# Performance work log

Measured on AMD Instinct MI355X. Metric: run time of the kernel, lower is better.

## Reference

```python
import math
import jax, jax.numpy as jnp
import numpy as np

B, T, T_P, C, H = 4, 2048, 256, 768, 12
HD = C // H


def setup_inputs() -> dict:
    key = jax.random.key(0)
    k1, k2, k3, k4 = jax.random.split(key, 4)
    x = jax.random.normal(k1, (B, T, C), dtype=jnp.float32)
    prefix = jax.random.normal(k2, (B, T_P, C), dtype=jnp.float32)
    # torch nn.Linear weight layout: (out_features, in_features)
    W_qkv = jax.random.normal(k3, (3 * C, C), dtype=jnp.float32) * (1.0 / math.sqrt(C))
    W_out = jax.random.normal(k4, (C, C), dtype=jnp.float32) * (1.0 / math.sqrt(C))
    return {"x": x, "prefix": prefix, "W_qkv": W_qkv, "W_out": W_out}


def _mac_causal_mask(t_p: int, t: int) -> jnp.ndarray:
    total = t_p + t
    mask = jnp.zeros((total, total), dtype=bool)
    mask = mask.at[:t_p, t_p:].set(True)  # h tokens blocked from x tokens
    causal = jnp.triu(jnp.ones((t, t), dtype=bool), k=1)  # causal within x block
    return mask.at[t_p:, t_p:].set(causal)


def reference(x, prefix, W_qkv, W_out):
    b, t, c = x.shape
    t_p = prefix.shape[1]
    t_all = t_p + t
    x_full = jnp.concatenate([prefix, x], axis=1)          # (B, T_all, C)
    qkv = x_full @ W_qkv.T                                  # (B, T_all, 3C)
    q, k, v = jnp.split(qkv, 3, axis=-1)
    # (B, H, T_all, HD)
    q = q.reshape(b, t_all, H, HD).transpose(0, 2, 1, 3)
    k = k.reshape(b, t_all, H, HD).transpose(0, 2, 1, 3)
    v = v.reshape(b, t_all, H, HD).transpose(0, 2, 1, 3)
    scale = 1.0 / math.sqrt(HD)
    att = jnp.einsum('bhqd,bhkd->bhqk', q, k) * scale       # (B, H, T_all, T_all)
    mask = _mac_causal_mask(t_p, t)
    att = jnp.where(mask[None, None], -jnp.inf, att)
    att = jax.nn.softmax(att, axis=-1)                      # dropout = identity (eval)
    out = jnp.einsum('bhqk,bhkd->bhqd', att, v)             # (B, H, T_all, HD)
    out = out.transpose(0, 2, 1, 3).reshape(b, t_all, c)
    out = out @ W_out.T
    return out[:, t_p:, :]                                  # only x portion (B, T, C)
```

## Files before the change

### kernel.cpp

```cpp
#include <hip/hip_runtime.h>

constexpr int Bn   = 4;
constexpr int Tn   = 2048;
constexpr int TPn  = 256;
constexpr int TALLn = 2304;
constexpr int Cn   = 768;
constexpr int Hn   = 12;
constexpr int HDn  = 64;

typedef __bf16 bf16x4 __attribute__((ext_vector_type(4)));
typedef __bf16 bf16x8 __attribute__((ext_vector_type(8)));
typedef float  f32x4  __attribute__((ext_vector_type(4)));
typedef unsigned u32x4 __attribute__((ext_vector_type(4)));

__device__ __forceinline__ unsigned short f2bf(float f) {
    unsigned int x = __float_as_uint(f);
    x += 0x7fffu + ((x >> 16) & 1u);
    return (unsigned short)(x >> 16);
}

__device__ __forceinline__ unsigned cvt_pk_bf16(float a, float b) {
    unsigned r;
    asm("v_cvt_pk_bf16_f32 %0, %1, %2" : "=v"(r) : "v"(a), "v"(b));
    return r;
}

#define ASYNC16(gsrc, ldst)                                                           \
    __builtin_amdgcn_global_load_lds((__attribute__((address_space(1))) void*)(gsrc), \
                                     (__attribute__((address_space(3))) void*)(ldst), \
                                     16, 0, 0)

__global__ __launch_bounds__(256) void k_build_xfull(
        const float* __restrict__ x, const float* __restrict__ pre,
        unsigned short* __restrict__ xf) {
    int idx = blockIdx.x * 256 + threadIdx.x;
    int row = idx / (Cn / 4);
    int c   = (idx - row * (Cn / 4)) * 4;
    int b = row / TALLn, tt = row - b * TALLn;
    const float* src = (tt < TPn) ? pre + ((size_t)b * TPn + tt) * Cn + c
                                  : x   + ((size_t)b * Tn + (tt - TPn)) * Cn + c;
    float4 f = *reinterpret_cast<const float4*>(src);
    ushort4 o = { f2bf(f.x), f2bf(f.y), f2bf(f.z), f2bf(f.w) };
    *reinterpret_cast<ushort4*>(xf + (size_t)row * Cn + c) = o;
}

__global__ __launch_bounds__(256) void k_cast2(
        const float* __restrict__ wqkv, const float* __restrict__ wout,
        unsigned short* __restrict__ wqb, unsigned short* __restrict__ wob) {
    int idx = (blockIdx.x * 256 + threadIdx.x) * 4;
    const int n1 = 3 * Cn * Cn;
    const float* src;
    unsigned short* dst;
    if (idx < n1) { src = wqkv + idx; dst = wqb + idx; }
    else          { src = wout + (idx - n1); dst = wob + (idx - n1); }
    float4 f = *reinterpret_cast<const float4*>(src);
    ushort4 o = { f2bf(f.x), f2bf(f.y), f2bf(f.z), f2bf(f.w) };
    *reinterpret_cast<ushort4*>(dst) = o;
}

__global__ __launch_bounds__(256) void k_qkv_gemm(
        const unsigned short* __restrict__ A, const unsigned short* __restrict__ W,
        unsigned short* __restrict__ Qb, unsigned short* __restrict__ Kb,
        unsigned short* __restrict__ Vt) {
    __shared__ __align__(16) unsigned short smem[16384];
    const int tid  = threadIdx.x;
    const int wave = tid >> 6;
    const int lane = tid & 63;
    const int g = lane >> 4, l16 = lane & 15;
    const int m0 = blockIdx.x * 128, n0 = blockIdx.y * 128;
    const int wr = wave >> 1, wc = wave & 1;

    const unsigned short* pa[2];
    const unsigned short* pb[2];
    int sd[2];
    #pragma unroll
    for (int inst = 0; inst < 2; ++inst) {
        const int li = inst * 256 + tid;
        const int row = li >> 2;
        const int ch = (li & 3) ^ ((row >> 1) & 3);
        pa[inst] = A + (size_t)(m0 + row) * Cn + ch * 8;
        pb[inst] = W + (size_t)(n0 + row) * Cn + ch * 8;
        sd[inst] = (inst * 256 + wave * 64) * 8;
    }
    int aoff[4], boff[4];
    #pragma unroll
    for (int mt = 0; mt < 4; ++mt) {
        const int ra = wr * 64 + mt * 16 + l16;
        aoff[mt] = ra * 32 + ((g ^ ((ra >> 1) & 3)) << 3);
        const int rb = wc * 64 + mt * 16 + l16;
        boff[mt] = rb * 32 + ((g ^ ((rb >> 1) & 3)) << 3);
    }

    f32x4 acc[4][4] = {};

    #pragma unroll
    for (int inst = 0; inst < 2; ++inst) {
        ASYNC16(pa[inst], &smem[0]    + sd[inst]);
        ASYNC16(pb[inst], &smem[8192] + sd[inst]);
        pa[inst] += 32;
        pb[inst] += 32;
    }
    __syncthreads();

    int buf = 0;
    for (int kk = 0; kk < 24; ++kk) {
        if (kk + 1 < 24) {
            #pragma unroll
            for (int inst = 0; inst < 2; ++inst) {
                ASYNC16(pa[inst], &smem[(buf ^ 1) * 4096]        + sd[inst]);
                ASYNC16(pb[inst], &smem[8192 + (buf ^ 1) * 4096] + sd[inst]);
                pa[inst] += 32;
                pb[inst] += 32;
            }
        }
        const unsigned short* Ab = &smem[buf * 4096];
        const unsigned short* Bb = &smem[8192 + buf * 4096];
        bf16x8 af[4], bfv[4];
        #pragma unroll
        for (int mt = 0; mt < 4; ++mt) {
            af[mt]  = *reinterpret_cast<const bf16x8*>(&Ab[aoff[mt]]);
            bfv[mt] = *reinterpret_cast<const bf16x8*>(&Bb[boff[mt]]);
        }
        __builtin_amdgcn_s_setprio(1);
        #pragma unroll
        for (int mt = 0; mt < 4; ++mt)
            #pragma unroll
            for (int nt = 0; nt < 4; ++nt)
                acc[mt][nt] = __builtin_amdgcn_mfma_f32_16x16x32_bf16(
                        af[mt], bfv[nt], acc[mt][nt], 0, 0, 0);
        __builtin_amdgcn_s_setprio(0);
        buf ^= 1;
        __syncthreads();
    }

    const int b   = m0 / TALLn;
    const int t0  = m0 - b * TALLn;
    const int sel = n0 / Cn;
    const int hn0 = n0 - sel * Cn;
    constexpr float SCQ = 0.18033688011112042f;

    if (sel == 2) {
        #pragma unroll
        for (int mt = 0; mt < 4; ++mt)
            #pragma unroll
            for (int nt = 0; nt < 4; ++nt)
                #pragma unroll
                for (int r = 0; r < 4; ++r) {
                    const int t  = wr * 64 + mt * 16 + g * 4 + r;
                    const int hn = wc * 64 + nt * 16 + l16;
                    smem[hn * 128 + (((t >> 3) ^ (hn & 7)) << 3) + (t & 7)] =
                            f2bf(acc[mt][nt][r]);
                }
        __syncthreads();
        #pragma unroll
        for (int j = 0; j < 8; ++j) {
            const int u  = tid + 256 * j;
            const int hn = u >> 4, tc = u & 15;
            const int tile64 = tc >> 3;
            const int np = tc & 7;
            const int kg = np >> 2, gs = np & 3;
            const int tgA = tile64 * 8 + kg * 4 + (gs >> 1);
            const int sub = (gs & 1) * 4;
            bf16x4 rA = *reinterpret_cast<const bf16x4*>(
                    &smem[hn * 128 + ((tgA ^ (hn & 7)) << 3) + sub]);
            bf16x4 rB = *reinterpret_cast<const bf16x4*>(
                    &smem[hn * 128 + (((tgA + 2) ^ (hn & 7)) << 3) + sub]);
            bf16x8 v = __builtin_shufflevector(rA, rB, 0, 1, 2, 3, 4, 5, 6, 7);
            const int hh = (hn0 + hn) >> 6;
            const int dd = hn & 63;
            *reinterpret_cast<bf16x8*>(
                    &Vt[(((size_t)b * Hn + hh) * HDn + dd) * TALLn + t0 + tc * 8]) = v;
        }
    } else {
        #pragma unroll
        for (int mt = 0; mt < 4; ++mt)
            #pragma unroll
            for (int nt = 0; nt < 4; ++nt)
                #pragma unroll
                for (int r = 0; r < 4; ++r) {
                    const int t  = t0 + wr * 64 + mt * 16 + g * 4 + r;
                    const int hn = hn0 + wc * 64 + nt * 16 + l16;
                    const int h = hn >> 6, d = hn & 63;
                    if (sel == 0)
                        Qb[(((size_t)b * Hn + h) * TALLn + t) * HDn + d] =
                                f2bf(acc[mt][nt][r] * SCQ);
                    else
                        Kb[(((size_t)b * Hn + h) * TALLn + t) * HDn + d] =
                                f2bf(acc[mt][nt][r]);
                }
    }
}

__global__ __launch_bounds__(256) void k_attn(
        const unsigned short* __restrict__ Qb, const unsigned short* __restrict__ Kb,
        const unsigned short* __restrict__ Vt, unsigned short* __restrict__ Ob) {
    __shared__ __align__(16) unsigned short Ks[2][4096];
    __shared__ __align__(16) unsigned short Vs[2][4096];
    const int tid  = threadIdx.x;
    const int wq   = tid >> 6;
    const int lane = tid & 63;
    const int l16  = lane & 15;
    const int g    = lane >> 4;

    const int fb  = blockIdx.x;
    const int j   = fb >> 3;
    const int bh  = 6 * (fb & 7) + (j % 6);
    const int chunk = 31 - (j / 6);
    const int nkt = 5 + chunk;
    const size_t kv = (size_t)bh * TALLn * HDn;

    int koff[4][2];
    #pragma unroll
    for (int band = 0; band < 4; ++band)
        #pragma unroll
        for (int ks = 0; ks < 2; ++ks)
            koff[band][ks] = (band * 16 + l16) * 64 + (((ks * 4 + g) ^ (l16 & 7)) << 3);
    int voff[2];
    #pragma unroll
    for (int kg = 0; kg < 2; ++kg)
        voff[kg] = l16 * 64 + (((kg * 4 + g) ^ (l16 & 7)) << 3);
    const unsigned short* pk[2];
    const unsigned short* pv[2];
    int sdst[2];
    #pragma unroll
    for (int inst = 0; inst < 2; ++inst) {
        const int li = inst * 256 + tid;
        const int row = li >> 3;
        const int ch = (li & 7) ^ (row & 7);
        pk[inst] = Kb + kv + row * HDn + ch * 8;
        pv[inst] = Vt + kv + row * TALLn + ch * 8;
        sdst[inst] = (inst * 256 + wq * 64) * 8;
    }
    constexpr int KSTRIDE = 64 * HDn;
    constexpr int VSTRIDE = 64;

    bf16x8 qf[2];
    {
        const int tq = TPn + chunk * 64 + wq * 16 + l16;
        #pragma unroll
        for (int ks = 0; ks < 2; ++ks)
            qf[ks] = *reinterpret_cast<const bf16x8*>(
                    Qb + kv + (size_t)tq * HDn + ks * 32 + g * 8);
    }

    bf16x8 ones;
    #pragma unroll
    for (int i = 0; i < 8; ++i) ones[i] = (__bf16)1.0f;

    f32x4 oacc[4] = {};
    f32x4 lacc = {};

    #pragma unroll
    for (int inst = 0; inst < 2; ++inst) {
        ASYNC16(pk[inst], &Ks[0][0] + sdst[inst]);
        ASYNC16(pv[inst], &Vs[0][0] + sdst[inst]);
        pk[inst] += KSTRIDE;
        pv[inst] += VSTRIDE;
    }
    __syncthreads();

    int buf = 0;
    for (int t = 0; t < nkt; ++t) {
        if (t + 1 < nkt) {
            #pragma unroll
            for (int inst = 0; inst < 2; ++inst) {
                ASYNC16(pk[inst], &Ks[buf ^ 1][0] + sdst[inst]);
                ASYNC16(pv[inst], &Vs[buf ^ 1][0] + sdst[inst]);
                pk[inst] += KSTRIDE;
                pv[inst] += VSTRIDE;
            }
        }
        const unsigned short* Ksb = &Ks[buf][0];
        const unsigned short* Vsb = &Vs[buf][0];

        f32x4 sacc[4] = {};
        __builtin_amdgcn_s_setprio(1);
        #pragma unroll
        for (int band = 0; band < 4; ++band) {
            bf16x8 k0 = *reinterpret_cast<const bf16x8*>(&Ksb[koff[band][0]]);
            bf16x8 k1 = *reinterpret_cast<const bf16x8*>(&Ksb[koff[band][1]]);
            sacc[band] = __builtin_amdgcn_mfma_f32_16x16x32_bf16(
                    k0, qf[0], sacc[band], 0, 0, 0);
            sacc[band] = __builtin_amdgcn_mfma_f32_16x16x32_bf16(
                    k1, qf[1], sacc[band], 0, 0, 0);
        }
        __builtin_amdgcn_s_setprio(0);

        if (t == nkt - 1) {
            const int lim = TPn + chunk * 64 + wq * 16 + l16 - t * 64;
            #pragma unroll
            for (int band = 0; band < 4; ++band)
                #pragma unroll
                for (int r = 0; r < 4; ++r)
                    sacc[band][r] = (band * 16 + g * 4 + r <= lim) ? sacc[band][r]
                                                                   : -1e30f;
        }
        unsigned dwb[4][2];
        #pragma unroll
        for (int band = 0; band < 4; ++band) {
            const float e0 = exp2f(sacc[band][0]);
            const float e1 = exp2f(sacc[band][1]);
            const float e2 = exp2f(sacc[band][2]);
            const float e3 = exp2f(sacc[band][3]);
            dwb[band][0] = cvt_pk_bf16(e0, e1);
            dwb[band][1] = cvt_pk_bf16(e2, e3);
        }

        __builtin_amdgcn_s_setprio(1);
        #pragma unroll
        for (int kg = 0; kg < 2; ++kg) {
            const u32x4 uu = { dwb[2 * kg][0], dwb[2 * kg][1],
                               dwb[2 * kg + 1][0], dwb[2 * kg + 1][1] };
            const bf16x8 pf = __builtin_bit_cast(bf16x8, uu);
            lacc = __builtin_amdgcn_mfma_f32_16x16x32_bf16(ones, pf, lacc, 0, 0, 0);
            #pragma unroll
            for (int dband = 0; dband < 4; ++dband) {
                bf16x8 vf = *reinterpret_cast<const bf16x8*>(
                        &Vsb[dband * 1024 + voff[kg]]);
                oacc[dband] = __builtin_amdgcn_mfma_f32_16x16x32_bf16(
                        vf, pf, oacc[dband], 0, 0, 0);
            }
        }
        __builtin_amdgcn_s_setprio(0);

        buf ^= 1;
        __syncthreads();
    }

    const int b = bh / Hn, h = bh - b * Hn;
    const float inv = 1.0f / lacc[0];
    const size_t row = (size_t)b * Tn + chunk * 64 + wq * 16 + l16;
    #pragma unroll
    for (int dband = 0; dband < 4; ++dband) {
        ushort4 st;
        st.x = f2bf(oacc[dband][0] * inv);
        st.y = f2bf(oacc[dband][1] * inv);
        st.z = f2bf(oacc[dband][2] * inv);
        st.w = f2bf(oacc[dband][3] * inv);
        *reinterpret_cast<ushort4*>(&Ob[row * Cn + h * 64 + dband * 16 + g * 4]) = st;
    }
}

__global__ __launch_bounds__(256) void k_out_gemm(
        const unsigned short* __restrict__ A, const unsigned short* __restrict__ W,
        float* __restrict__ out) {
    __shared__ __align__(16) unsigned short smem[16384];
    const int tid  = threadIdx.x;
    const int wave = tid >> 6;
    const int lane = tid & 63;
    const int g = lane >> 4, l16 = lane & 15;
    const int m0 = blockIdx.x * 128, n0 = blockIdx.y * 128;
    const int wr = wave >> 1, wc = wave & 1;

    const unsigned short* pa[2];
    const unsigned short* pb[2];
    int sd[2];
    #pragma unroll
    for (int inst = 0; inst < 2; ++inst) {
        const int li = inst * 256 + tid;
        const int row = li >> 2;
        const int ch = (li & 3) ^ ((row >> 1) & 3);
        pa[inst] = A + (size_t)(m0 + row) * Cn + ch * 8;
        pb[inst] = W + (size_t)(n0 + row) * Cn + ch * 8;
        sd[inst] = (inst * 256 + wave * 64) * 8;
    }
    int aoff[4], boff[4];
    #pragma unroll
    for (int mt = 0; mt < 4; ++mt) {
        const int ra = wr * 64 + mt * 16 + l16;
        aoff[mt] = ra * 32 + ((g ^ ((ra >> 1) & 3)) << 3);
        const int rb = wc * 64 + mt * 16 + l16;
        boff[mt] = rb * 32 + ((g ^ ((rb >> 1) & 3)) << 3);
    }

    f32x4 acc[4][4] = {};

    #pragma unroll
    for (int inst = 0; inst < 2; ++inst) {
        ASYNC16(pa[inst], &smem[0]    + sd[inst]);
        ASYNC16(pb[inst], &smem[8192] + sd[inst]);
        pa[inst] += 32;
        pb[inst] += 32;
    }
    __syncthreads();

    int buf = 0;
    for (int kk = 0; kk < 24; ++kk) {
        if (kk + 1 < 24) {
            #pragma unroll
            for (int inst = 0; inst < 2; ++inst) {
                ASYNC16(pa[inst], &smem[(buf ^ 1) * 4096]        + sd[inst]);
                ASYNC16(pb[inst], &smem[8192 + (buf ^ 1) * 4096] + sd[inst]);
                pa[inst] += 32;
                pb[inst] += 32;
            }
        }
        const unsigned short* Ab = &smem[buf * 4096];
        const unsigned short* Bb = &smem[8192 + buf * 4096];
        bf16x8 af[4], bfv[4];
        #pragma unroll
        for (int mt = 0; mt < 4; ++mt) {
            af[mt]  = *reinterpret_cast<const bf16x8*>(&Ab[aoff[mt]]);
            bfv[mt] = *reinterpret_cast<const bf16x8*>(&Bb[boff[mt]]);
        }
        __builtin_amdgcn_s_setprio(1);
        #pragma unroll
        for (int mt = 0; mt < 4; ++mt)
            #pragma unroll
            for (int nt = 0; nt < 4; ++nt)
                acc[mt][nt] = __builtin_amdgcn_mfma_f32_16x16x32_bf16(
                        af[mt], bfv[nt], acc[mt][nt], 0, 0, 0);
        __builtin_amdgcn_s_setprio(0);
        buf ^= 1;
        __syncthreads();
    }

    #pragma unroll
    for (int mt = 0; mt < 4; ++mt)
        #pragma unroll
        for (int nt = 0; nt < 4; ++nt)
            #pragma unroll
            for (int r = 0; r < 4; ++r) {
                const int m = m0 + wr * 64 + mt * 16 + g * 4 + r;
                const int n = n0 + wc * 64 + nt * 16 + l16;
                out[(size_t)m * Cn + n] = acc[mt][nt][r];
            }
}

extern "C" void kernel_launch(void* const* d_in, const int* in_sizes, int n_in,
                              void* d_out, int out_size, void* d_ws, size_t ws_size,
                              hipStream_t stream) {
    const float* x    = (const float*)d_in[0];
    const float* pre  = (const float*)d_in[1];
    const float* wqkv = (const float*)d_in[2];
    const float* wout = (const float*)d_in[3];
    float* out = (float*)d_out;
    char* ws = (char*)d_ws;

    unsigned short* xf  = (unsigned short*)(ws + 0);
    unsigned short* wqb = (unsigned short*)(ws + 14155776);
    unsigned short* wob = (unsigned short*)(ws + 17694720);
    unsigned short* Qb  = (unsigned short*)(ws + 18874368);
    unsigned short* Kb  = (unsigned short*)(ws + 33030144);
    unsigned short* Vt  = (unsigned short*)(ws + 47185920);
    unsigned short* Ob  = (unsigned short*)(ws + 61341696);

    k_build_xfull<<<dim3((Bn * TALLn * Cn / 4) / 256), 256, 0, stream>>>(x, pre, xf);
    k_cast2<<<dim3((4 * Cn * Cn / 4) / 256), 256, 0, stream>>>(wqkv, wout, wqb, wob);
    k_qkv_gemm<<<dim3((Bn * TALLn) / 128, (3 * Cn) / 128), 256, 0, stream>>>(
            xf, wqb, Qb, Kb, Vt);
    k_attn<<<dim3(1536), 256, 0, stream>>>(Qb, Kb, Vt, Ob);
    k_out_gemm<<<dim3((Bn * Tn) / 128, Cn / 128), 256, 0, stream>>>(Ob, wob, out);
}
```

Baseline: 141.2 us.

## Merge cast kernels and give each attention wave two query tiles

The two fp32-to-bf16 cast kernels are merged into one prep launch to remove a kernel launch. The attention kernel drops from 4 waves to 2 waves per block, and each wave now handles 32 query rows as two 16-row tiles. Each K/V fragment read from LDS therefore feeds twice as many MFMAs, cutting LDS traffic per unit of compute. The cost is higher register pressure and fewer waves per block for latency hiding, plus each thread now issues twice as many async loads.

```diff
diff --git a/kernel.cpp b/kernel.cpp
--- a/kernel.cpp
+++ b/kernel.cpp
@@ -30,29 +30,28 @@
                                      (__attribute__((address_space(3))) void*)(ldst), \
                                      16, 0, 0)
 
-__global__ __launch_bounds__(256) void k_build_xfull(
+__global__ __launch_bounds__(256) void k_prep(
         const float* __restrict__ x, const float* __restrict__ pre,
-        unsigned short* __restrict__ xf) {
-    int idx = blockIdx.x * 256 + threadIdx.x;
-    int row = idx / (Cn / 4);
-    int c   = (idx - row * (Cn / 4)) * 4;
-    int b = row / TALLn, tt = row - b * TALLn;
-    const float* src = (tt < TPn) ? pre + ((size_t)b * TPn + tt) * Cn + c
-                                  : x   + ((size_t)b * Tn + (tt - TPn)) * Cn + c;
-    float4 f = *reinterpret_cast<const float4*>(src);
-    ushort4 o = { f2bf(f.x), f2bf(f.y), f2bf(f.z), f2bf(f.w) };
-    *reinterpret_cast<ushort4*>(xf + (size_t)row * Cn + c) = o;
-}
-
-__global__ __launch_bounds__(256) void k_cast2(
         const float* __restrict__ wqkv, const float* __restrict__ wout,
-        unsigned short* __restrict__ wqb, unsigned short* __restrict__ wob) {
-    int idx = (blockIdx.x * 256 + threadIdx.x) * 4;
-    const int n1 = 3 * Cn * Cn;
+        unsigned short* __restrict__ xf, unsigned short* __restrict__ wqb,
+        unsigned short* __restrict__ wob) {
+    const int idx = blockIdx.x * 256 + threadIdx.x;
+    constexpr int NXF = Bn * TALLn * Cn / 4;
+    constexpr int NW1 = 3 * Cn * Cn / 4;
     const float* src;
     unsigned short* dst;
-    if (idx < n1) { src = wqkv + idx; dst = wqb + idx; }
-    else          { src = wout + (idx - n1); dst = wob + (idx - n1); }
+    if (idx < NXF) {
+        const int row = idx / (Cn / 4);
+        const int c   = (idx - row * (Cn / 4)) * 4;
+        const int b = row / TALLn, tt = row - b * TALLn;
+        src = (tt < TPn) ? pre + ((size_t)b * TPn + tt) * Cn + c
+                         : x   + ((size_t)b * Tn + (tt - TPn)) * Cn + c;
+        dst = xf + (size_t)row * Cn + c;
+    } else {
+        const int k = idx - NXF;
+        if (k < NW1) { src = wqkv + (size_t)k * 4; dst = wqb + (size_t)k * 4; }
+        else { src = wout + (size_t)(k - NW1) * 4; dst = wob + (size_t)(k - NW1) * 4; }
+    }
     float4 f = *reinterpret_cast<const float4*>(src);
     ushort4 o = { f2bf(f.x), f2bf(f.y), f2bf(f.z), f2bf(f.w) };
     *reinterpret_cast<ushort4*>(dst) = o;
@@ -191,13 +190,13 @@
     }
 }
 
-__global__ __launch_bounds__(256) void k_attn(
+__global__ __launch_bounds__(128) void k_attn(
         const unsigned short* __restrict__ Qb, const unsigned short* __restrict__ Kb,
         const unsigned short* __restrict__ Vt, unsigned short* __restrict__ Ob) {
     __shared__ __align__(16) unsigned short Ks[2][4096];
     __shared__ __align__(16) unsigned short Vs[2][4096];
     const int tid  = threadIdx.x;
-    const int wq   = tid >> 6;
+    const int wave = tid >> 6;
     const int lane = tid & 63;
     const int l16  = lane & 15;
     const int g    = lane >> 4;
@@ -219,39 +218,42 @@
     #pragma unroll
     for (int kg = 0; kg < 2; ++kg)
         voff[kg] = l16 * 64 + (((kg * 4 + g) ^ (l16 & 7)) << 3);
-    const unsigned short* pk[2];
-    const unsigned short* pv[2];
-    int sdst[2];
-    #pragma unroll
-    for (int inst = 0; inst < 2; ++inst) {
-        const int li = inst * 256 + tid;
+    const unsigned short* pk[4];
+    const unsigned short* pv[4];
+    int sdst[4];
+    #pragma unroll
+    for (int inst = 0; inst < 4; ++inst) {
+        const int li = inst * 128 + tid;
         const int row = li >> 3;
         const int ch = (li & 7) ^ (row & 7);
         pk[inst] = Kb + kv + row * HDn + ch * 8;
         pv[inst] = Vt + kv + row * TALLn + ch * 8;
-        sdst[inst] = (inst * 256 + wq * 64) * 8;
+        sdst[inst] = (inst * 128 + wave * 64) * 8;
     }
     constexpr int KSTRIDE = 64 * HDn;
     constexpr int VSTRIDE = 64;
 
-    bf16x8 qf[2];
+    bf16x8 qfA[2], qfB[2];
     {
-        const int tq = TPn + chunk * 64 + wq * 16 + l16;
-        #pragma unroll
-        for (int ks = 0; ks < 2; ++ks)
-            qf[ks] = *reinterpret_cast<const bf16x8*>(
+        const int tq = TPn + chunk * 64 + wave * 32 + l16;
+        #pragma unroll
+        for (int ks = 0; ks < 2; ++ks) {
+            qfA[ks] = *reinterpret_cast<const bf16x8*>(
                     Qb + kv + (size_t)tq * HDn + ks * 32 + g * 8);
+            qfB[ks] = *reinterpret_cast<const bf16x8*>(
+                    Qb + kv + (size_t)(tq + 16) * HDn + ks * 32 + g * 8);
+        }
     }
 
     bf16x8 ones;
     #pragma unroll
     for (int i = 0; i < 8; ++i) ones[i] = (__bf16)1.0f;
 
-    f32x4 oacc[4] = {};
-    f32x4 lacc = {};
-
-    #pragma unroll
-    for (int inst = 0; inst < 2; ++inst) {
+    f32x4 oaccA[4] = {}, oaccB[4] = {};
+    f32x4 laccA = {}, laccB = {};
+
+    #pragma unroll
+    for (int inst = 0; inst < 4; ++inst) {
         ASYNC16(pk[inst], &Ks[0][0] + sdst[inst]);
         ASYNC16(pv[inst], &Vs[0][0] + sdst[inst]);
         pk[inst] += KSTRIDE;
@@ -263,7 +265,7 @@
     for (int t = 0; t < nkt; ++t) {
         if (t + 1 < nkt) {
             #pragma unroll
-            for (int inst = 0; inst < 2; ++inst) {
+            for (int inst = 0; inst < 4; ++inst) {
                 ASYNC16(pk[inst], &Ks[buf ^ 1][0] + sdst[inst]);
                 ASYNC16(pv[inst], &Vs[buf ^ 1][0] + sdst[inst]);
                 pk[inst] += KSTRIDE;
@@ -273,52 +275,59 @@
         const unsigned short* Ksb = &Ks[buf][0];
         const unsigned short* Vsb = &Vs[buf][0];
 
-        f32x4 sacc[4] = {};
+        f32x4 sA[4] = {}, sB[4] = {};
         __builtin_amdgcn_s_setprio(1);
         #pragma unroll
         for (int band = 0; band < 4; ++band) {
             bf16x8 k0 = *reinterpret_cast<const bf16x8*>(&Ksb[koff[band][0]]);
             bf16x8 k1 = *reinterpret_cast<const bf16x8*>(&Ksb[koff[band][1]]);
-            sacc[band] = __builtin_amdgcn_mfma_f32_16x16x32_bf16(
-                    k0, qf[0], sacc[band], 0, 0, 0);
-            sacc[band] = __builtin_amdgcn_mfma_f32_16x16x32_bf16(
-                    k1, qf[1], sacc[band], 0, 0, 0);
+            sA[band] = __builtin_amdgcn_mfma_f32_16x16x32_bf16(k0, qfA[0], sA[band], 0, 0, 0);
+            sA[band] = __builtin_amdgcn_mfma_f32_16x16x32_bf16(k1, qfA[1], sA[band], 0, 0, 0);
+            sB[band] = __builtin_amdgcn_mfma_f32_16x16x32_bf16(k0, qfB[0], sB[band], 0, 0, 0);
+            sB[band] = __builtin_amdgcn_mfma_f32_16x16x32_bf16(k1, qfB[1], sB[band], 0, 0, 0);
         }
         __builtin_amdgcn_s_setprio(0);
 
         if (t == nkt - 1) {
-            const int lim = TPn + chunk * 64 + wq * 16 + l16 - t * 64;
+            const int limA = wave * 32 + l16;
             #pragma unroll
             for (int band = 0; band < 4; ++band)
                 #pragma unroll
-                for (int r = 0; r < 4; ++r)
-                    sacc[band][r] = (band * 16 + g * 4 + r <= lim) ? sacc[band][r]
-                                                                   : -1e30f;
-        }
-        unsigned dwb[4][2];
+                for (int r = 0; r < 4; ++r) {
+                    const int key = band * 16 + g * 4 + r;
+                    sA[band][r] = (key <= limA)      ? sA[band][r] : -1e30f;
+                    sB[band][r] = (key <= limA + 16) ? sB[band][r] : -1e30f;
+                }
+        }
+
+        unsigned dwA[4][2], dwB[4][2];
         #pragma unroll
         for (int band = 0; band < 4; ++band) {
-            const float e0 = exp2f(sacc[band][0]);
-            const float e1 = exp2f(sacc[band][1]);
-            const float e2 = exp2f(sacc[band][2]);
-            const float e3 = exp2f(sacc[band][3]);
-            dwb[band][0] = cvt_pk_bf16(e0, e1);
-            dwb[band][1] = cvt_pk_bf16(e2, e3);
+            dwA[band][0] = cvt_pk_bf16(exp2f(sA[band][0]), exp2f(sA[band][1]));
+            dwA[band][1] = cvt_pk_bf16(exp2f(sA[band][2]), exp2f(sA[band][3]));
+            dwB[band][0] = cvt_pk_bf16(exp2f(sB[band][0]), exp2f(sB[band][1]));
+            dwB[band][1] = cvt_pk_bf16(exp2f(sB[band][2]), exp2f(sB[band][3]));
         }
 
         __builtin_amdgcn_s_setprio(1);
         #pragma unroll
         for (int kg = 0; kg < 2; ++kg) {
-            const u32x4 uu = { dwb[2 * kg][0], dwb[2 * kg][1],
-                               dwb[2 * kg + 1][0], dwb[2 * kg + 1][1] };
-            const bf16x8 pf = __builtin_bit_cast(bf16x8, uu);
-            lacc = __builtin_amdgcn_mfma_f32_16x16x32_bf16(ones, pf, lacc, 0, 0, 0);
+            const u32x4 uA = { dwA[2 * kg][0], dwA[2 * kg][1],
+                               dwA[2 * kg + 1][0], dwA[2 * kg + 1][1] };
+            const u32x4 uB = { dwB[2 * kg][0], dwB[2 * kg][1],
+                               dwB[2 * kg + 1][0], dwB[2 * kg + 1][1] };
+            const bf16x8 pfA = __builtin_bit_cast(bf16x8, uA);
+            const bf16x8 pfB = __builtin_bit_cast(bf16x8, uB);
+            laccA = __builtin_amdgcn_mfma_f32_16x16x32_bf16(ones, pfA, laccA, 0, 0, 0);
+            laccB = __builtin_amdgcn_mfma_f32_16x16x32_bf16(ones, pfB, laccB, 0, 0, 0);
             #pragma unroll
             for (int dband = 0; dband < 4; ++dband) {
                 bf16x8 vf = *reinterpret_cast<const bf16x8*>(
                         &Vsb[dband * 1024 + voff[kg]]);
-                oacc[dband] = __builtin_amdgcn_mfma_f32_16x16x32_bf16(
-                        vf, pf, oacc[dband], 0, 0, 0);
+                oaccA[dband] = __builtin_amdgcn_mfma_f32_16x16x32_bf16(
+                        vf, pfA, oaccA[dband], 0, 0, 0);
+                oaccB[dband] = __builtin_amdgcn_mfma_f32_16x16x32_bf16(
+                        vf, pfB, oaccB[dband], 0, 0, 0);
             }
         }
         __builtin_amdgcn_s_setprio(0);
@@ -328,16 +337,22 @@
     }
 
     const int b = bh / Hn, h = bh - b * Hn;
-    const float inv = 1.0f / lacc[0];
-    const size_t row = (size_t)b * Tn + chunk * 64 + wq * 16 + l16;
+    const float invA = 1.0f / laccA[0];
+    const float invB = 1.0f / laccB[0];
+    const size_t rowA = (size_t)b * Tn + chunk * 64 + wave * 32 + l16;
     #pragma unroll
     for (int dband = 0; dband < 4; ++dband) {
         ushort4 st;
-        st.x = f2bf(oacc[dband][0] * inv);
-        st.y = f2bf(oacc[dband][1] * inv);
-        st.z = f2bf(oacc[dband][2] * inv);
-        st.w = f2bf(oacc[dband][3] * inv);
-        *reinterpret_cast<ushort4*>(&Ob[row * Cn + h * 64 + dband * 16 + g * 4]) = st;
+        st.x = f2bf(oaccA[dband][0] * invA);
+        st.y = f2bf(oaccA[dband][1] * invA);
+        st.z = f2bf(oaccA[dband][2] * invA);
+        st.w = f2bf(oaccA[dband][3] * invA);
+        *reinterpret_cast<ushort4*>(&Ob[rowA * Cn + h * 64 + dband * 16 + g * 4]) = st;
+        st.x = f2bf(oaccB[dband][0] * invB);
+        st.y = f2bf(oaccB[dband][1] * invB);
+        st.z = f2bf(oaccB[dband][2] * invB);
+        st.w = f2bf(oaccB[dband][3] * invB);
+        *reinterpret_cast<ushort4*>(&Ob[(rowA + 16) * Cn + h * 64 + dband * 16 + g * 4]) = st;
     }
 }
 
@@ -445,10 +460,10 @@
     unsigned short* Vt  = (unsigned short*)(ws + 47185920);
     unsigned short* Ob  = (unsigned short*)(ws + 61341696);
 
-    k_build_xfull<<<dim3((Bn * TALLn * Cn / 4) / 256), 256, 0, stream>>>(x, pre, xf);
-    k_cast2<<<dim3((4 * Cn * Cn / 4) / 256), 256, 0, stream>>>(wqkv, wout, wqb, wob);
+    constexpr int PREP_UNITS = (Bn * TALLn * Cn + 4 * Cn * Cn) / 4;
+    k_prep<<<dim3(PREP_UNITS / 256), 256, 0, stream>>>(x, pre, wqkv, wout, xf, wqb, wob);
     k_qkv_gemm<<<dim3((Bn * TALLn) / 128, (3 * Cn) / 128), 256, 0, stream>>>(
             xf, wqb, Qb, Kb, Vt);
-    k_attn<<<dim3(1536), 256, 0, stream>>>(Qb, Kb, Vt, Ob);
+    k_attn<<<dim3(1536), 128, 0, stream>>>(Qb, Kb, Vt, Ob);
     k_out_gemm<<<dim3((Bn * Tn) / 128, Cn / 128), 256, 0, stream>>>(Ob, wob, out);
 }
```

Result: slower. 158.6 us (+12.3%).

## Triple-buffer attention K/V staging and merge input cast kernels

Applied to the files above, without the earlier changes.

The attention kernel moves from double to triple buffering of K/V tiles in LDS. It prefetches two tiles ahead and uses explicit vmcnt waits with a single barrier per iteration, replacing the full __syncthreads, so more global-to-LDS latency can be hidden. The two fp32-to-bf16 prep kernels are also fused into one launch to save launch overhead. The cost is more LDS per block, which may lower occupancy. The causal mask limit expression is simplified, since it is equivalent on the last tile.

```diff
diff --git a/kernel.cpp b/kernel.cpp
--- a/kernel.cpp
+++ b/kernel.cpp
@@ -30,29 +30,28 @@
                                      (__attribute__((address_space(3))) void*)(ldst), \
                                      16, 0, 0)
 
-__global__ __launch_bounds__(256) void k_build_xfull(
+__global__ __launch_bounds__(256) void k_prep(
         const float* __restrict__ x, const float* __restrict__ pre,
-        unsigned short* __restrict__ xf) {
-    int idx = blockIdx.x * 256 + threadIdx.x;
-    int row = idx / (Cn / 4);
-    int c   = (idx - row * (Cn / 4)) * 4;
-    int b = row / TALLn, tt = row - b * TALLn;
-    const float* src = (tt < TPn) ? pre + ((size_t)b * TPn + tt) * Cn + c
-                                  : x   + ((size_t)b * Tn + (tt - TPn)) * Cn + c;
-    float4 f = *reinterpret_cast<const float4*>(src);
-    ushort4 o = { f2bf(f.x), f2bf(f.y), f2bf(f.z), f2bf(f.w) };
-    *reinterpret_cast<ushort4*>(xf + (size_t)row * Cn + c) = o;
-}
-
-__global__ __launch_bounds__(256) void k_cast2(
         const float* __restrict__ wqkv, const float* __restrict__ wout,
-        unsigned short* __restrict__ wqb, unsigned short* __restrict__ wob) {
-    int idx = (blockIdx.x * 256 + threadIdx.x) * 4;
-    const int n1 = 3 * Cn * Cn;
+        unsigned short* __restrict__ xf, unsigned short* __restrict__ wqb,
+        unsigned short* __restrict__ wob) {
+    const int idx = blockIdx.x * 256 + threadIdx.x;
+    constexpr int NXF = Bn * TALLn * Cn / 4;
+    constexpr int NW1 = 3 * Cn * Cn / 4;
     const float* src;
     unsigned short* dst;
-    if (idx < n1) { src = wqkv + idx; dst = wqb + idx; }
-    else          { src = wout + (idx - n1); dst = wob + (idx - n1); }
+    if (idx < NXF) {
+        const int row = idx / (Cn / 4);
+        const int c   = (idx - row * (Cn / 4)) * 4;
+        const int b = row / TALLn, tt = row - b * TALLn;
+        src = (tt < TPn) ? pre + ((size_t)b * TPn + tt) * Cn + c
+                         : x   + ((size_t)b * Tn + (tt - TPn)) * Cn + c;
+        dst = xf + (size_t)row * Cn + c;
+    } else {
+        const int k = idx - NXF;
+        if (k < NW1) { src = wqkv + (size_t)k * 4; dst = wqb + (size_t)k * 4; }
+        else { src = wout + (size_t)(k - NW1) * 4; dst = wob + (size_t)(k - NW1) * 4; }
+    }
     float4 f = *reinterpret_cast<const float4*>(src);
     ushort4 o = { f2bf(f.x), f2bf(f.y), f2bf(f.z), f2bf(f.w) };
     *reinterpret_cast<ushort4*>(dst) = o;
@@ -194,8 +193,8 @@
 __global__ __launch_bounds__(256) void k_attn(
         const unsigned short* __restrict__ Qb, const unsigned short* __restrict__ Kb,
         const unsigned short* __restrict__ Vt, unsigned short* __restrict__ Ob) {
-    __shared__ __align__(16) unsigned short Ks[2][4096];
-    __shared__ __align__(16) unsigned short Vs[2][4096];
+    __shared__ __align__(16) unsigned short Ks[3][4096];
+    __shared__ __align__(16) unsigned short Vs[3][4096];
     const int tid  = threadIdx.x;
     const int wq   = tid >> 6;
     const int lane = tid & 63;
@@ -234,6 +233,16 @@
     constexpr int KSTRIDE = 64 * HDn;
     constexpr int VSTRIDE = 64;
 
+    auto stageKV = [&](int bs) {
+        #pragma unroll
+        for (int inst = 0; inst < 2; ++inst) {
+            ASYNC16(pk[inst], &Ks[bs][0] + sdst[inst]);
+            ASYNC16(pv[inst], &Vs[bs][0] + sdst[inst]);
+            pk[inst] += KSTRIDE;
+            pv[inst] += VSTRIDE;
+        }
+    };
+
     bf16x8 qf[2];
     {
         const int tq = TPn + chunk * 64 + wq * 16 + l16;
@@ -250,28 +259,21 @@
     f32x4 oacc[4] = {};
     f32x4 lacc = {};
 
-    #pragma unroll
-    for (int inst = 0; inst < 2; ++inst) {
-        ASYNC16(pk[inst], &Ks[0][0] + sdst[inst]);
-        ASYNC16(pv[inst], &Vs[0][0] + sdst[inst]);
-        pk[inst] += KSTRIDE;
-        pv[inst] += VSTRIDE;
-    }
-    __syncthreads();
-
-    int buf = 0;
+    stageKV(0);
+    stageKV(1);
+    asm volatile("s_waitcnt vmcnt(4)" ::: "memory");
+    __builtin_amdgcn_sched_barrier(0);
+    __builtin_amdgcn_s_barrier();
+    __builtin_amdgcn_sched_barrier(0);
+
+    int cur = 0;
     for (int t = 0; t < nkt; ++t) {
-        if (t + 1 < nkt) {
-            #pragma unroll
-            for (int inst = 0; inst < 2; ++inst) {
-                ASYNC16(pk[inst], &Ks[buf ^ 1][0] + sdst[inst]);
-                ASYNC16(pv[inst], &Vs[buf ^ 1][0] + sdst[inst]);
-                pk[inst] += KSTRIDE;
-                pv[inst] += VSTRIDE;
-            }
-        }
-        const unsigned short* Ksb = &Ks[buf][0];
-        const unsigned short* Vsb = &Vs[buf][0];
+        if (t + 2 < nkt) {
+            const int nb = (cur + 2 >= 3) ? cur - 1 : cur + 2;
+            stageKV(nb);
+        }
+        const unsigned short* Ksb = &Ks[cur][0];
+        const unsigned short* Vsb = &Vs[cur][0];
 
         f32x4 sacc[4] = {};
         __builtin_amdgcn_s_setprio(1);
@@ -287,7 +289,7 @@
         __builtin_amdgcn_s_setprio(0);
 
         if (t == nkt - 1) {
-            const int lim = TPn + chunk * 64 + wq * 16 + l16 - t * 64;
+            const int lim = wq * 16 + l16;
             #pragma unroll
             for (int band = 0; band < 4; ++band)
                 #pragma unroll
@@ -323,8 +325,16 @@
         }
         __builtin_amdgcn_s_setprio(0);
 
-        buf ^= 1;
-        __syncthreads();
+        if (t + 1 < nkt) {
+            if (t + 2 < nkt)
+                asm volatile("s_waitcnt vmcnt(4)" ::: "memory");
+            else
+                asm volatile("s_waitcnt vmcnt(0)" ::: "memory");
+            __builtin_amdgcn_sched_barrier(0);
+            __builtin_amdgcn_s_barrier();
+            __builtin_amdgcn_sched_barrier(0);
+            cur = (cur + 1 >= 3) ? 0 : cur + 1;
+        }
     }
 
     const int b = bh / Hn, h = bh - b * Hn;
@@ -445,8 +455,8 @@
     unsigned short* Vt  = (unsigned short*)(ws + 47185920);
     unsigned short* Ob  = (unsigned short*)(ws + 61341696);
 
-    k_build_xfull<<<dim3((Bn * TALLn * Cn / 4) / 256), 256, 0, stream>>>(x, pre, xf);
-    k_cast2<<<dim3((4 * Cn * Cn / 4) / 256), 256, 0, stream>>>(wqkv, wout, wqb, wob);
+    constexpr int PREP_UNITS = (Bn * TALLn * Cn + 4 * Cn * Cn) / 4;
+    k_prep<<<dim3(PREP_UNITS / 256), 256, 0, stream>>>(x, pre, wqkv, wout, xf, wqb, wob);
     k_qkv_gemm<<<dim3((Bn * TALLn) / 128, (3 * Cn) / 128), 256, 0, stream>>>(
             xf, wqb, Qb, Kb, Vt);
     k_attn<<<dim3(1536), 256, 0, stream>>>(Qb, Kb, Vt, Ob);
```

Result: no change. 143.9 us (+2.0%).
